# Kernel tuning notes

Measured on AMD Instinct MI355X. Metric: run time of the kernel, lower is better.

The kernel has to match this reference:

```python
import jax, jax.numpy as jnp
import numpy as np

N_NODES = 50000
N_EDGES = 800000
IN_SIZE = 128
NUM_HEADS = 8
HEAD_DIM = IN_SIZE // NUM_HEADS  # qk/val head dim = 16


def setup_inputs() -> dict:
    key = jax.random.key(0)
    ks = jax.random.split(key, 16)
    d = IN_SIZE
    lim = 1.0 / np.sqrt(d)
    inp = {
        "in_feats": jax.random.normal(ks[0], (N_NODES, d), jnp.float32),
        "struc_feats": jax.random.normal(ks[1], (N_NODES, d), jnp.float32),
        "edge_weights": jax.random.uniform(ks[2], (N_EDGES,), jnp.float32),
        "ln_scale": jnp.ones((d,), jnp.float32),
        "ln_bias": jnp.zeros((d,), jnp.float32),
        "Ws": jax.random.uniform(ks[3], (d, d), jnp.float32, -lim, lim),
        "bs": jnp.zeros((d,), jnp.float32),
        "Wq": jax.random.uniform(ks[4], (d, d), jnp.float32, -lim, lim),
        "bq": jnp.zeros((d,), jnp.float32),
        "Wk": jax.random.uniform(ks[5], (d, d), jnp.float32, -lim, lim),
        "bk": jnp.zeros((d,), jnp.float32),
        "Wv": jax.random.uniform(ks[6], (d, d), jnp.float32, -lim, lim),
        "bv": jnp.zeros((d,), jnp.float32),
        "Wo": jax.random.uniform(ks[7], (d, d), jnp.float32, -lim, lim),
        "edge_ids": jax.random.randint(ks[8], (2, N_EDGES), 0, N_NODES, jnp.int64)
        if jax.config.jax_enable_x64 else jax.random.randint(ks[8], (2, N_EDGES), 0, N_NODES, jnp.int32),
    }
    return inp


def _layer_norm(x, scale, bias, eps=1e-5):
    mu = jnp.mean(x, axis=-1, keepdims=True)
    var = jnp.var(x, axis=-1, keepdims=True)
    return (x - mu) * jax.lax.rsqrt(var + eps) * scale + bias


def reference(in_feats, struc_feats, edge_weights, ln_scale, ln_bias,
              Ws, bs, Wq, bq, Wk, bk, Wv, bv, Wo, edge_ids):
    N = in_feats.shape[0]
    H, hd = NUM_HEADS, HEAD_DIM

    delta = _layer_norm(in_feats, ln_scale, ln_bias)           # pre-norm
    delta = jax.nn.gelu(delta, approximate=False)               # pre-activation (exact GELU, torch default)
    delta_struc = delta + struc_feats @ Ws.T + bs               # struc_proj add

    qry = (delta_struc @ Wq.T + bq) / np.sqrt(hd)                # [N, qk]
    keyf = delta_struc @ Wk.T + bk                               # [N, qk]
    val = delta @ Wv.T + bv                                      # [N, val]

    src, dst = edge_ids[0], edge_ids[1]                          # out[src] += A[src,dst] * val[dst]
    qe = qry[src].reshape(-1, H, hd)                             # [E, H, hd]
    ke = keyf[dst].reshape(-1, H, hd)                            # [E, H, hd]
    attn = jax.nn.sigmoid(jnp.sum(qe * ke, axis=-1))             # [E, H]
    attn = edge_weights[:, None] * attn

    msgs = attn[:, :, None] * val[dst].reshape(-1, H, hd)        # [E, H, hd]
    agg = jax.ops.segment_sum(msgs.reshape(-1, H * hd), src, num_segments=N)  # [N, val]

    out = agg @ Wo.T                                             # out_proj (no bias)
    return in_feats + out                                        # skip connection
```

## Files before the change

### kernel.cpp

```cpp
#include <hip/hip_runtime.h>
#include <math.h>

#define NF 128

typedef __attribute__((ext_vector_type(8))) short short8;
typedef __attribute__((ext_vector_type(4))) float floatx4;

__device__ __forceinline__ unsigned short f2bf(float f) {
    union { float x; unsigned int i; } c; c.x = f;
    unsigned int r = c.i + 0x7fffu + ((c.i >> 16) & 1u);
    return (unsigned short)(r >> 16);
}
__device__ __forceinline__ float bf2f(unsigned short u) {
    union { unsigned int i; float x; } c; c.i = ((unsigned int)u) << 16;
    return c.x;
}
__device__ __forceinline__ void unpack8(uint4 u, float* f) {
    union { unsigned int i; float x; } c;
    c.i = u.x << 16;          f[0] = c.x;
    c.i = u.x & 0xffff0000u;  f[1] = c.x;
    c.i = u.y << 16;          f[2] = c.x;
    c.i = u.y & 0xffff0000u;  f[3] = c.x;
    c.i = u.z << 16;          f[4] = c.x;
    c.i = u.z & 0xffff0000u;  f[5] = c.x;
    c.i = u.w << 16;          f[6] = c.x;
    c.i = u.w & 0xffff0000u;  f[7] = c.x;
}
__device__ __forceinline__ ushort4 pack4(float a, float b, float c, float d) {
    ushort4 h; h.x = f2bf(a); h.y = f2bf(b); h.z = f2bf(c); h.w = f2bf(d);
    return h;
}

__global__ __launch_bounds__(256) void wconv5_kernel(
    const float* __restrict__ a, const float* __restrict__ b,
    const float* __restrict__ c, const float* __restrict__ d,
    const float* __restrict__ e, unsigned short* __restrict__ o)
{
    int i = blockIdx.x * 256 + threadIdx.x;
    int w = i >> 14, j = i & 16383;
    const float* p = (w == 0) ? a : (w == 1) ? b : (w == 2) ? c : (w == 3) ? d : e;
    o[i] = f2bf(p[j]);
}

__global__ __launch_bounds__(256) void node_a_kernel(
    const float* __restrict__ in_feats, const float* __restrict__ struc,
    const float* __restrict__ gamma, const float* __restrict__ beta,
    const unsigned short* __restrict__ Wsb, const float* __restrict__ bs,
    unsigned short* __restrict__ deltab, unsigned short* __restrict__ dstrb, int M)
{
    __shared__ unsigned short Xd[64][136];
    __shared__ unsigned short Xs2[64][136];
    __shared__ unsigned short Wl[64][136];

    int tid = threadIdx.x;
    int m0 = blockIdx.x * 64;
    int lane = tid & 63, w = tid >> 6, lg = lane & 15, quad = lane >> 4;

    {
        const uint4* g = (const uint4*)Wsb;
        #pragma unroll
        for (int p = 0; p < 4; ++p) {
            int idx = tid + p * 256;
            *(uint4*)&Wl[idx >> 4][(idx & 15) * 8] = g[idx];
        }
    }
    {
        int row = tid >> 2, t4 = tid & 3;
        int gm = m0 + row;
        bool vr = gm < M;
        const float4* ip = (const float4*)(in_feats + (size_t)gm * NF) + t4 * 8;
        float4 xf[8];
        #pragma unroll
        for (int p = 0; p < 8; ++p)
            xf[p] = vr ? ip[p] : make_float4(0.f, 0.f, 0.f, 0.f);
        float s = 0.f, sq = 0.f;
        #pragma unroll
        for (int p = 0; p < 8; ++p) {
            s  += xf[p].x + xf[p].y + xf[p].z + xf[p].w;
            sq += xf[p].x * xf[p].x + xf[p].y * xf[p].y
                + xf[p].z * xf[p].z + xf[p].w * xf[p].w;
        }
        s  += __shfl_xor(s, 1, 64);  s  += __shfl_xor(s, 2, 64);
        sq += __shfl_xor(sq, 1, 64); sq += __shfl_xor(sq, 2, 64);
        float mu = s * (1.0f / 128.0f);
        float var = sq * (1.0f / 128.0f) - mu * mu;
        float rstd = rsqrtf(var + 1e-5f);
        const float4* gp = (const float4*)gamma + t4 * 8;
        const float4* bp = (const float4*)beta + t4 * 8;
        #pragma unroll
        for (int p = 0; p < 8; ++p) {
            float4 g4 = gp[p], b4 = bp[p];
            float o0 = (xf[p].x - mu) * rstd * g4.x + b4.x;
            float o1 = (xf[p].y - mu) * rstd * g4.y + b4.y;
            float o2 = (xf[p].z - mu) * rstd * g4.z + b4.z;
            float o3 = (xf[p].w - mu) * rstd * g4.w + b4.w;
            o0 = 0.5f * o0 * (1.0f + erff(o0 * 0.70710678118654752f));
            o1 = 0.5f * o1 * (1.0f + erff(o1 * 0.70710678118654752f));
            o2 = 0.5f * o2 * (1.0f + erff(o2 * 0.70710678118654752f));
            o3 = 0.5f * o3 * (1.0f + erff(o3 * 0.70710678118654752f));
            *(ushort4*)&Xd[row][t4 * 32 + p * 4] = pack4(o0, o1, o2, o3);
        }
        const float4* sp = (const float4*)(struc + (size_t)gm * NF) + t4 * 8;
        #pragma unroll
        for (int p = 0; p < 8; ++p) {
            float4 f = vr ? sp[p] : make_float4(0.f, 0.f, 0.f, 0.f);
            *(ushort4*)&Xs2[row][t4 * 32 + p * 4] = pack4(f.x, f.y, f.z, f.w);
        }
    }
    __syncthreads();

    floatx4 acc[8];
    #pragma unroll
    for (int t = 0; t < 8; ++t) acc[t] = (floatx4){0.f, 0.f, 0.f, 0.f};

    #pragma unroll
    for (int ks = 0; ks < 4; ++ks) {
        short8 a = *(const short8*)&Xs2[w * 16 + lg][ks * 32 + quad * 8];
        #pragma unroll
        for (int t = 0; t < 4; ++t) {
            short8 b = *(const short8*)&Wl[t * 16 + lg][ks * 32 + quad * 8];
            acc[t] = __builtin_amdgcn_mfma_f32_16x16x32_bf16(a, b, acc[t], 0, 0, 0);
        }
    }
    __syncthreads();
    {
        const uint4* g = (const uint4*)(Wsb + 8192);
        #pragma unroll
        for (int p = 0; p < 4; ++p) {
            int idx = tid + p * 256;
            *(uint4*)&Wl[idx >> 4][(idx & 15) * 8] = g[idx];
        }
    }
    __syncthreads();
    #pragma unroll
    for (int ks = 0; ks < 4; ++ks) {
        short8 a = *(const short8*)&Xs2[w * 16 + lg][ks * 32 + quad * 8];
        #pragma unroll
        for (int t = 0; t < 4; ++t) {
            short8 b = *(const short8*)&Wl[t * 16 + lg][ks * 32 + quad * 8];
            acc[4 + t] = __builtin_amdgcn_mfma_f32_16x16x32_bf16(a, b, acc[4 + t], 0, 0, 0);
        }
    }

    #pragma unroll
    for (int t = 0; t < 8; ++t) {
        int col = t * 16 + lg;
        float bvv = bs[col];
        #pragma unroll
        for (int r = 0; r < 4; ++r) {
            int rl = w * 16 + quad * 4 + r;
            Xs2[rl][col] = f2bf(acc[t][r] + bvv + bf2f(Xd[rl][col]));
        }
    }
    #pragma unroll
    for (int p = 0; p < 4; ++p) {
        int idx = lane + p * 64;
        int row = w * 16 + (idx >> 4), c16 = idx & 15;
        int gm = m0 + row;
        if (gm < M) {
            *(uint4*)(deltab + (size_t)gm * NF + c16 * 8) = *(const uint4*)&Xd[row][c16 * 8];
            *(uint4*)(dstrb  + (size_t)gm * NF + c16 * 8) = *(const uint4*)&Xs2[row][c16 * 8];
        }
    }
}

__global__ __launch_bounds__(256) void node_qkv_kernel(
    const unsigned short* __restrict__ deltab, const unsigned short* __restrict__ dstrb,
    const unsigned short* __restrict__ Wall, const float* __restrict__ bq,
    const float* __restrict__ bk, const float* __restrict__ bv,
    unsigned short* __restrict__ qb, unsigned short* __restrict__ kb,
    unsigned short* __restrict__ vb, int M)
{
    __shared__ unsigned short Xs[64][136];
    __shared__ unsigned short Wl[128][136];

    int tid = threadIdx.x;
    int m0 = blockIdx.x * 64;
    int y = blockIdx.y;
    int lane = tid & 63, w = tid >> 6, lg = lane & 15, quad = lane >> 4;

    const unsigned short* Xg = (y == 2) ? deltab : dstrb;
    const unsigned short* Wg = Wall + (y + 1) * 16384;
    const float* bias = (y == 0) ? bq : (y == 1) ? bk : bv;
    float scale = (y == 0) ? 0.25f : 1.0f;
    unsigned short* outg = (y == 0) ? qb : (y == 1) ? kb : vb;

    {
        const uint4* g = (const uint4*)Wg;
        #pragma unroll
        for (int p = 0; p < 8; ++p) {
            int idx = tid + p * 256;
            *(uint4*)&Wl[idx >> 4][(idx & 15) * 8] = g[idx];
        }
    }
    {
        const uint4* X = (const uint4*)Xg;
        #pragma unroll
        for (int p = 0; p < 4; ++p) {
            int idx = lane + p * 64;
            int row = w * 16 + (idx >> 4), c16 = idx & 15;
            int gm = m0 + row;
            uint4 u = make_uint4(0u, 0u, 0u, 0u);
            if (gm < M) u = X[(size_t)gm * 16 + c16];
            *(uint4*)&Xs[row][c16 * 8] = u;
        }
    }
    __syncthreads();

    floatx4 acc[8];
    #pragma unroll
    for (int t = 0; t < 8; ++t) acc[t] = (floatx4){0.f, 0.f, 0.f, 0.f};
    #pragma unroll
    for (int ks = 0; ks < 4; ++ks) {
        short8 a = *(const short8*)&Xs[w * 16 + lg][ks * 32 + quad * 8];
        #pragma unroll
        for (int t = 0; t < 8; ++t) {
            short8 b = *(const short8*)&Wl[t * 16 + lg][ks * 32 + quad * 8];
            acc[t] = __builtin_amdgcn_mfma_f32_16x16x32_bf16(a, b, acc[t], 0, 0, 0);
        }
    }

    #pragma unroll
    for (int t = 0; t < 8; ++t) {
        int col = t * 16 + lg;
        float bvv = bias[col];
        #pragma unroll
        for (int r = 0; r < 4; ++r)
            Xs[w * 16 + quad * 4 + r][col] = f2bf((acc[t][r] + bvv) * scale);
    }
    #pragma unroll
    for (int p = 0; p < 4; ++p) {
        int idx = lane + p * 64;
        int row = w * 16 + (idx >> 4), c16 = idx & 15;
        int gm = m0 + row;
        if (gm < M)
            *(uint4*)(outg + (size_t)gm * NF + c16 * 8) = *(const uint4*)&Xs[row][c16 * 8];
    }
}

__global__ __launch_bounds__(256) void gemm_out_kernel(
    const unsigned short* __restrict__ Xb, const unsigned short* __restrict__ Wb,
    const float* __restrict__ addf, float* __restrict__ Y, int M)
{
    __shared__ unsigned short Xs[64][136];
    __shared__ unsigned short Wl[128][136];
    int tid = threadIdx.x;
    int m0 = blockIdx.x * 64;
    int lane = tid & 63, w = tid >> 6, lg = lane & 15, quad = lane >> 4;

    {
        const uint4* g = (const uint4*)Wb;
        #pragma unroll
        for (int p = 0; p < 8; ++p) {
            int idx = tid + p * 256;
            *(uint4*)&Wl[idx >> 4][(idx & 15) * 8] = g[idx];
        }
    }
    {
        const uint4* X = (const uint4*)Xb;
        #pragma unroll
        for (int p = 0; p < 4; ++p) {
            int idx = lane + p * 64;
            int row = w * 16 + (idx >> 4), c16 = idx & 15;
            int gm = m0 + row;
            uint4 u = make_uint4(0u, 0u, 0u, 0u);
            if (gm < M) u = X[(size_t)gm * 16 + c16];
            *(uint4*)&Xs[row][c16 * 8] = u;
        }
    }
    __syncthreads();

    floatx4 acc[8];
    #pragma unroll
    for (int t = 0; t < 8; ++t) acc[t] = (floatx4){0.f, 0.f, 0.f, 0.f};
    #pragma unroll
    for (int ks = 0; ks < 4; ++ks) {
        short8 a = *(const short8*)&Xs[w * 16 + lg][ks * 32 + quad * 8];
        #pragma unroll
        for (int t = 0; t < 8; ++t) {
            short8 b = *(const short8*)&Wl[t * 16 + lg][ks * 32 + quad * 8];
            acc[t] = __builtin_amdgcn_mfma_f32_16x16x32_bf16(a, b, acc[t], 0, 0, 0);
        }
    }
    #pragma unroll
    for (int t = 0; t < 8; ++t) {
        int col = t * 16 + lg;
        #pragma unroll
        for (int r = 0; r < 4; ++r) {
            int gm = m0 + w * 16 + quad * 4 + r;
            if (gm >= M) continue;
            size_t off = (size_t)gm * NF + col;
            Y[off] = acc[t][r] + addf[off];
        }
    }
}

__global__ void hist_kernel(const int* __restrict__ eid, int* __restrict__ cnt, int E)
{
    int i = blockIdx.x * blockDim.x + threadIdx.x;
    if (i < E) atomicAdd(&cnt[eid[i]], 1);
}

__global__ __launch_bounds__(256) void scan1_kernel(
    const int* __restrict__ cnt, int* __restrict__ bsum, int n)
{
    int base = blockIdx.x * 1024;
    int s = 0;
    #pragma unroll
    for (int p = 0; p < 4; ++p) {
        int i = base + (int)threadIdx.x + p * 256;
        if (i < n) s += cnt[i];
    }
    #pragma unroll
    for (int m = 1; m <= 32; m <<= 1) s += __shfl_xor(s, m, 64);
    __shared__ int ws_[4];
    int wid = threadIdx.x >> 6;
    if ((threadIdx.x & 63) == 0) ws_[wid] = s;
    __syncthreads();
    if (threadIdx.x == 0) bsum[blockIdx.x] = ws_[0] + ws_[1] + ws_[2] + ws_[3];
}

__global__ __launch_bounds__(256) void scan3_kernel(
    const int* __restrict__ cnt, const int* __restrict__ bsum,
    int* __restrict__ row_start, int* __restrict__ cursor, int n, int nb)
{
    __shared__ int base_off;
    int tid = threadIdx.x, lane = tid & 63, wid = tid >> 6;
    if (tid == 0) {
        int a = 0;
        for (int j = 0; j < (int)blockIdx.x; ++j) a += bsum[j];
        base_off = a;
        if ((int)blockIdx.x == nb - 1) {
            int tot = a;
            for (int j = blockIdx.x; j < nb; ++j) tot += bsum[j];
            row_start[n] = tot;
        }
    }
    int base = blockIdx.x * 1024;
    int v[4]; int s = 0;
    #pragma unroll
    for (int p = 0; p < 4; ++p) {
        int i = base + tid * 4 + p;
        v[p] = (i < n) ? cnt[i] : 0;
        s += v[p];
    }
    int ss = s;
    #pragma unroll
    for (int off = 1; off < 64; off <<= 1) {
        int t = __shfl_up(ss, off, 64);
        if (lane >= off) ss += t;
    }
    __shared__ int wsum[4];
    if (lane == 63) wsum[wid] = ss;
    __syncthreads();
    int woff = 0;
    for (int j = 0; j < wid; ++j) woff += wsum[j];
    int a = base_off + woff + (ss - s);
    #pragma unroll
    for (int p = 0; p < 4; ++p) {
        int i = base + tid * 4 + p;
        if (i < n) { row_start[i] = a; cursor[i] = a; a += v[p]; }
    }
}

__global__ void scatter_kernel(const int* __restrict__ eid, const float* __restrict__ ew,
                               int* __restrict__ cursor, int2* __restrict__ edata, int E)
{
    int i = blockIdx.x * blockDim.x + threadIdx.x;
    if (i < E) {
        int src = eid[i];
        int dst = eid[E + i];
        int pos = atomicAdd(&cursor[src], 1);
        edata[pos] = make_int2(dst, __float_as_int(ew[i]));
    }
}

__global__ __launch_bounds__(256) void aggregate_kernel(
    const unsigned short* __restrict__ Q, const unsigned short* __restrict__ Kf,
    const unsigned short* __restrict__ V, const int* __restrict__ row_start,
    const int2* __restrict__ edata, unsigned short* __restrict__ agg, int N)
{
    int node = blockIdx.x * 4 + (threadIdx.x >> 6);
    if (node >= N) return;
    int lane = threadIdx.x & 63;
    int sg = lane >> 4, lg = lane & 15;
    int rs = row_start[node], re = row_start[node + 1];

    float qv[8];
    unpack8(*(const uint4*)(Q + (size_t)node * NF + lg * 8), qv);
    float acc[8];
    #pragma unroll
    for (int j = 0; j < 8; ++j) acc[j] = 0.f;

    int e1 = rs + sg, e2 = rs + sg + 4;
    int2 ed1 = (e1 < re) ? edata[e1] : make_int2(0, 0);
    int2 ed2 = (e2 < re) ? edata[e2] : make_int2(0, 0);

    for (int e0 = rs; e0 < re; e0 += 8) {
        int2 c1 = ed1, c2 = ed2;
        int en1 = e0 + 8 + sg, en2 = en1 + 4;
        ed1 = (en1 < re) ? edata[en1] : make_int2(0, 0);
        ed2 = (en2 < re) ? edata[en2] : make_int2(0, 0);

        float kv1[8], kv2[8];
        unpack8(*(const uint4*)(Kf + (size_t)c1.x * NF + lg * 8), kv1);
        unpack8(*(const uint4*)(Kf + (size_t)c2.x * NF + lg * 8), kv2);
        float s1 = qv[0] * kv1[0], s2 = qv[0] * kv2[0];
        #pragma unroll
        for (int j = 1; j < 8; ++j) {
            s1 = fmaf(qv[j], kv1[j], s1);
            s2 = fmaf(qv[j], kv2[j], s2);
        }
        s1 += __shfl_xor(s1, 1, 64);
        s2 += __shfl_xor(s2, 1, 64);
        float a1 = __int_as_float(c1.y) / (1.f + __expf(-s1));
        float a2 = __int_as_float(c2.y) / (1.f + __expf(-s2));

        float vv1[8], vv2[8];
        unpack8(*(const uint4*)(V + (size_t)c1.x * NF + lg * 8), vv1);
        unpack8(*(const uint4*)(V + (size_t)c2.x * NF + lg * 8), vv2);
        #pragma unroll
        for (int j = 0; j < 8; ++j) {
            acc[j] = fmaf(a1, vv1[j], acc[j]);
            acc[j] = fmaf(a2, vv2[j], acc[j]);
        }
    }
    #pragma unroll
    for (int j = 0; j < 8; ++j) {
        acc[j] += __shfl_xor(acc[j], 16, 64);
        acc[j] += __shfl_xor(acc[j], 32, 64);
    }
    if (sg == 0) {
        unsigned short* o = agg + (size_t)node * NF + lg * 8;
        *(ushort4*)o       = pack4(acc[0], acc[1], acc[2], acc[3]);
        *(ushort4*)(o + 4) = pack4(acc[4], acc[5], acc[6], acc[7]);
    }
}

extern "C" void kernel_launch(void* const* d_in, const int* in_sizes, int n_in,
                              void* d_out, int out_size, void* d_ws, size_t ws_size,
                              hipStream_t stream)
{
    const float* in_feats = (const float*)d_in[0];
    const float* struc    = (const float*)d_in[1];
    const float* eweights = (const float*)d_in[2];
    const float* ln_scale = (const float*)d_in[3];
    const float* ln_bias  = (const float*)d_in[4];
    const float* Ws       = (const float*)d_in[5];
    const float* bs       = (const float*)d_in[6];
    const float* Wq       = (const float*)d_in[7];
    const float* bq       = (const float*)d_in[8];
    const float* Wk       = (const float*)d_in[9];
    const float* bk       = (const float*)d_in[10];
    const float* Wv       = (const float*)d_in[11];
    const float* bv       = (const float*)d_in[12];
    const float* Wo       = (const float*)d_in[13];
    const int*   edge_ids = (const int*)d_in[14];
    float* out = (float*)d_out;

    int N = in_sizes[0] / NF;
    int E = in_sizes[2];

    size_t F = (size_t)N * NF;
    unsigned short* deltab = (unsigned short*)d_ws;
    unsigned short* dstrb  = deltab + F;
    unsigned short* qb     = dstrb + F;
    unsigned short* kb     = qb + F;
    unsigned short* vb     = kb + F;
    unsigned short* aggb   = vb + F;
    unsigned short* Wall   = aggb + F;
    int2*  edata     = (int2*)(Wall + 5 * 16384);
    int*   cnt       = (int*)(edata + E);
    int*   row_start = cnt + N;
    int*   cursor    = row_start + N + 1;
    int*   bsum      = cursor + N;

    int gb  = (N + 63) / 64;
    int geb = (E + 255) / 256;
    int nb  = (N + 1023) / 1024;

    wconv5_kernel<<<(5 * 16384) / 256, 256, 0, stream>>>(Ws, Wq, Wk, Wv, Wo, Wall);

    hipMemsetAsync(cnt, 0, (size_t)N * sizeof(int), stream);
    hist_kernel<<<geb, 256, 0, stream>>>(edge_ids, cnt, E);
    scan1_kernel<<<nb, 256, 0, stream>>>(cnt, bsum, N);
    scan3_kernel<<<nb, 256, 0, stream>>>(cnt, bsum, row_start, cursor, N, nb);
    scatter_kernel<<<geb, 256, 0, stream>>>(edge_ids, eweights, cursor, edata, E);

    node_a_kernel<<<gb, 256, 0, stream>>>(in_feats, struc, ln_scale, ln_bias,
                                          Wall, bs, deltab, dstrb, N);
    node_qkv_kernel<<<dim3(gb, 3), 256, 0, stream>>>(deltab, dstrb, Wall,
                                                     bq, bk, bv, qb, kb, vb, N);

    aggregate_kernel<<<(N + 3) / 4, 256, 0, stream>>>(qb, kb, vb, row_start, edata, aggb, N);

    gemm_out_kernel<<<gb, 256, 0, stream>>>(aggb, Wall + 4 * 16384, in_feats, out, N);
}
```

Measured before the change: 337.5 us.

## Persistent-tile GEMM kernels with resident weights and interleaved K/V layout

Turns the node GEMM kernels into persistent grid-stride loops, so each block loads the 128x128 bf16 weight matrix into LDS once and reuses it across many 64-row tiles. A operands now go straight from global memory into registers instead of being staged through LDS. K and V are stored interleaved per node, so the aggregation gathers both from one 512-byte row and gets better locality on random neighbor accesses. Costs include fixed grid sizes tuned to the device, more LDS per block in node_a, and missing barriers between tile iterations that reuse Xs2/Cst, which could race.

```diff
diff --git a/kernel.cpp b/kernel.cpp
--- a/kernel.cpp
+++ b/kernel.cpp
@@ -46,120 +46,118 @@
     const float* __restrict__ in_feats, const float* __restrict__ struc,
     const float* __restrict__ gamma, const float* __restrict__ beta,
     const unsigned short* __restrict__ Wsb, const float* __restrict__ bs,
-    unsigned short* __restrict__ deltab, unsigned short* __restrict__ dstrb, int M)
-{
-    __shared__ unsigned short Xd[64][136];
+    unsigned short* __restrict__ deltab, unsigned short* __restrict__ dstrb,
+    int M, int nt)
+{
+    __shared__ unsigned short Wl[128][136];
     __shared__ unsigned short Xs2[64][136];
-    __shared__ unsigned short Wl[64][136];
 
     int tid = threadIdx.x;
-    int m0 = blockIdx.x * 64;
     int lane = tid & 63, w = tid >> 6, lg = lane & 15, quad = lane >> 4;
+    int lrow = tid >> 2, t4 = tid & 3;
 
     {
         const uint4* g = (const uint4*)Wsb;
         #pragma unroll
-        for (int p = 0; p < 4; ++p) {
+        for (int p = 0; p < 8; ++p) {
             int idx = tid + p * 256;
             *(uint4*)&Wl[idx >> 4][(idx & 15) * 8] = g[idx];
         }
     }
-    {
-        int row = tid >> 2, t4 = tid & 3;
-        int gm = m0 + row;
+    float bsr[8];
+    #pragma unroll
+    for (int t = 0; t < 8; ++t) bsr[t] = bs[t * 16 + lg];
+    __syncthreads();
+
+    for (int tile = blockIdx.x; tile < nt; tile += gridDim.x) {
+        int m0 = tile * 64;
+        int gm = m0 + lrow;
         bool vr = gm < M;
-        const float4* ip = (const float4*)(in_feats + (size_t)gm * NF) + t4 * 8;
-        float4 xf[8];
-        #pragma unroll
-        for (int p = 0; p < 8; ++p)
-            xf[p] = vr ? ip[p] : make_float4(0.f, 0.f, 0.f, 0.f);
-        float s = 0.f, sq = 0.f;
-        #pragma unroll
-        for (int p = 0; p < 8; ++p) {
-            s  += xf[p].x + xf[p].y + xf[p].z + xf[p].w;
-            sq += xf[p].x * xf[p].x + xf[p].y * xf[p].y
-                + xf[p].z * xf[p].z + xf[p].w * xf[p].w;
-        }
-        s  += __shfl_xor(s, 1, 64);  s  += __shfl_xor(s, 2, 64);
-        sq += __shfl_xor(sq, 1, 64); sq += __shfl_xor(sq, 2, 64);
-        float mu = s * (1.0f / 128.0f);
-        float var = sq * (1.0f / 128.0f) - mu * mu;
-        float rstd = rsqrtf(var + 1e-5f);
-        const float4* gp = (const float4*)gamma + t4 * 8;
-        const float4* bp = (const float4*)beta + t4 * 8;
-        #pragma unroll
-        for (int p = 0; p < 8; ++p) {
-            float4 g4 = gp[p], b4 = bp[p];
-            float o0 = (xf[p].x - mu) * rstd * g4.x + b4.x;
-            float o1 = (xf[p].y - mu) * rstd * g4.y + b4.y;
-            float o2 = (xf[p].z - mu) * rstd * g4.z + b4.z;
-            float o3 = (xf[p].w - mu) * rstd * g4.w + b4.w;
-            o0 = 0.5f * o0 * (1.0f + erff(o0 * 0.70710678118654752f));
-            o1 = 0.5f * o1 * (1.0f + erff(o1 * 0.70710678118654752f));
-            o2 = 0.5f * o2 * (1.0f + erff(o2 * 0.70710678118654752f));
-            o3 = 0.5f * o3 * (1.0f + erff(o3 * 0.70710678118654752f));
-            *(ushort4*)&Xd[row][t4 * 32 + p * 4] = pack4(o0, o1, o2, o3);
-        }
-        const float4* sp = (const float4*)(struc + (size_t)gm * NF) + t4 * 8;
-        #pragma unroll
-        for (int p = 0; p < 8; ++p) {
-            float4 f = vr ? sp[p] : make_float4(0.f, 0.f, 0.f, 0.f);
-            *(ushort4*)&Xs2[row][t4 * 32 + p * 4] = pack4(f.x, f.y, f.z, f.w);
-        }
-    }
-    __syncthreads();
-
-    floatx4 acc[8];
-    #pragma unroll
-    for (int t = 0; t < 8; ++t) acc[t] = (floatx4){0.f, 0.f, 0.f, 0.f};
-
-    #pragma unroll
-    for (int ks = 0; ks < 4; ++ks) {
-        short8 a = *(const short8*)&Xs2[w * 16 + lg][ks * 32 + quad * 8];
-        #pragma unroll
-        for (int t = 0; t < 4; ++t) {
-            short8 b = *(const short8*)&Wl[t * 16 + lg][ks * 32 + quad * 8];
-            acc[t] = __builtin_amdgcn_mfma_f32_16x16x32_bf16(a, b, acc[t], 0, 0, 0);
-        }
-    }
-    __syncthreads();
-    {
-        const uint4* g = (const uint4*)(Wsb + 8192);
+        size_t rbase = (size_t)(vr ? gm : 0) * NF;
+
+        uint dreg[16];
+        {
+            const float4* ip = (const float4*)(in_feats + rbase) + t4 * 8;
+            float4 xf[8];
+            #pragma unroll
+            for (int p = 0; p < 8; ++p) xf[p] = ip[p];
+            float s = 0.f, sq = 0.f;
+            #pragma unroll
+            for (int p = 0; p < 8; ++p) {
+                s  += xf[p].x + xf[p].y + xf[p].z + xf[p].w;
+                sq += xf[p].x * xf[p].x + xf[p].y * xf[p].y
+                    + xf[p].z * xf[p].z + xf[p].w * xf[p].w;
+            }
+            s  += __shfl_xor(s, 1, 64);  s  += __shfl_xor(s, 2, 64);
+            sq += __shfl_xor(sq, 1, 64); sq += __shfl_xor(sq, 2, 64);
+            float mu = s * (1.0f / 128.0f);
+            float var = sq * (1.0f / 128.0f) - mu * mu;
+            float rstd = rsqrtf(var + 1e-5f);
+            const float4* gp = (const float4*)gamma + t4 * 8;
+            const float4* bp = (const float4*)beta + t4 * 8;
+            #pragma unroll
+            for (int p = 0; p < 8; ++p) {
+                float4 g4 = gp[p], b4 = bp[p];
+                float o0 = (xf[p].x - mu) * rstd * g4.x + b4.x;
+                float o1 = (xf[p].y - mu) * rstd * g4.y + b4.y;
+                float o2 = (xf[p].z - mu) * rstd * g4.z + b4.z;
+                float o3 = (xf[p].w - mu) * rstd * g4.w + b4.w;
+                o0 = 0.5f * o0 * (1.0f + erff(o0 * 0.70710678118654752f));
+                o1 = 0.5f * o1 * (1.0f + erff(o1 * 0.70710678118654752f));
+                o2 = 0.5f * o2 * (1.0f + erff(o2 * 0.70710678118654752f));
+                o3 = 0.5f * o3 * (1.0f + erff(o3 * 0.70710678118654752f));
+                ushort4 h = pack4(o0, o1, o2, o3);
+                dreg[p * 2]     = (uint)h.x | ((uint)h.y << 16);
+                dreg[p * 2 + 1] = (uint)h.z | ((uint)h.w << 16);
+            }
+            if (vr) {
+                uint4* od = (uint4*)(deltab + (size_t)gm * NF + t4 * 32);
+                #pragma unroll
+                for (int q = 0; q < 4; ++q)
+                    od[q] = make_uint4(dreg[q*4], dreg[q*4+1], dreg[q*4+2], dreg[q*4+3]);
+            }
+            const float4* sp = (const float4*)(struc + rbase) + t4 * 8;
+            #pragma unroll
+            for (int p = 0; p < 8; ++p) {
+                float4 f = sp[p];
+                *(ushort4*)&Xs2[lrow][t4 * 32 + p * 4] = pack4(f.x, f.y, f.z, f.w);
+            }
+        }
+
+        floatx4 acc[8];
+        #pragma unroll
+        for (int t = 0; t < 8; ++t) acc[t] = (floatx4){0.f, 0.f, 0.f, 0.f};
+        #pragma unroll
+        for (int ks = 0; ks < 4; ++ks) {
+            short8 a = *(const short8*)&Xs2[w * 16 + lg][ks * 32 + quad * 8];
+            #pragma unroll
+            for (int t = 0; t < 8; ++t) {
+                short8 b = *(const short8*)&Wl[t * 16 + lg][ks * 32 + quad * 8];
+                acc[t] = __builtin_amdgcn_mfma_f32_16x16x32_bf16(a, b, acc[t], 0, 0, 0);
+            }
+        }
+
+        #pragma unroll
+        for (int q = 0; q < 4; ++q)
+            *(uint4*)&Xs2[lrow][t4 * 32 + q * 8] =
+                make_uint4(dreg[q*4], dreg[q*4+1], dreg[q*4+2], dreg[q*4+3]);
+
+        #pragma unroll
+        for (int t = 0; t < 8; ++t) {
+            int col = t * 16 + lg;
+            #pragma unroll
+            for (int r = 0; r < 4; ++r) {
+                int rl = w * 16 + quad * 4 + r;
+                Xs2[rl][col] = f2bf(acc[t][r] + bsr[t] + bf2f(Xs2[rl][col]));
+            }
+        }
         #pragma unroll
         for (int p = 0; p < 4; ++p) {
-            int idx = tid + p * 256;
-            *(uint4*)&Wl[idx >> 4][(idx & 15) * 8] = g[idx];
-        }
-    }
-    __syncthreads();
-    #pragma unroll
-    for (int ks = 0; ks < 4; ++ks) {
-        short8 a = *(const short8*)&Xs2[w * 16 + lg][ks * 32 + quad * 8];
-        #pragma unroll
-        for (int t = 0; t < 4; ++t) {
-            short8 b = *(const short8*)&Wl[t * 16 + lg][ks * 32 + quad * 8];
-            acc[4 + t] = __builtin_amdgcn_mfma_f32_16x16x32_bf16(a, b, acc[4 + t], 0, 0, 0);
-        }
-    }
-
-    #pragma unroll
-    for (int t = 0; t < 8; ++t) {
-        int col = t * 16 + lg;
-        float bvv = bs[col];
-        #pragma unroll
-        for (int r = 0; r < 4; ++r) {
-            int rl = w * 16 + quad * 4 + r;
-            Xs2[rl][col] = f2bf(acc[t][r] + bvv + bf2f(Xd[rl][col]));
-        }
-    }
-    #pragma unroll
-    for (int p = 0; p < 4; ++p) {
-        int idx = lane + p * 64;
-        int row = w * 16 + (idx >> 4), c16 = idx & 15;
-        int gm = m0 + row;
-        if (gm < M) {
-            *(uint4*)(deltab + (size_t)gm * NF + c16 * 8) = *(const uint4*)&Xd[row][c16 * 8];
-            *(uint4*)(dstrb  + (size_t)gm * NF + c16 * 8) = *(const uint4*)&Xs2[row][c16 * 8];
+            int idx = lane + p * 64;
+            int row = w * 16 + (idx >> 4), c16 = idx & 15;
+            int gmo = m0 + row;
+            if (gmo < M)
+                *(uint4*)(dstrb + (size_t)gmo * NF + c16 * 8) = *(const uint4*)&Xs2[row][c16 * 8];
         }
     }
 }
@@ -168,14 +166,13 @@
     const unsigned short* __restrict__ deltab, const unsigned short* __restrict__ dstrb,
     const unsigned short* __restrict__ Wall, const float* __restrict__ bq,
     const float* __restrict__ bk, const float* __restrict__ bv,
-    unsigned short* __restrict__ qb, unsigned short* __restrict__ kb,
-    unsigned short* __restrict__ vb, int M)
-{
-    __shared__ unsigned short Xs[64][136];
+    unsigned short* __restrict__ qb, unsigned short* __restrict__ kvb,
+    int M, int nt)
+{
     __shared__ unsigned short Wl[128][136];
+    __shared__ unsigned short Cst[64][136];
 
     int tid = threadIdx.x;
-    int m0 = blockIdx.x * 64;
     int y = blockIdx.y;
     int lane = tid & 63, w = tid >> 6, lg = lane & 15, quad = lane >> 4;
 
@@ -183,7 +180,8 @@
     const unsigned short* Wg = Wall + (y + 1) * 16384;
     const float* bias = (y == 0) ? bq : (y == 1) ? bk : bv;
     float scale = (y == 0) ? 0.25f : 1.0f;
-    unsigned short* outg = (y == 0) ? qb : (y == 1) ? kb : vb;
+    unsigned short* outg = (y == 0) ? qb : (y == 1) ? kvb : (kvb + NF);
+    int ostride = (y == 0) ? NF : 2 * NF;
 
     {
         const uint4* g = (const uint4*)Wg;
@@ -193,59 +191,54 @@
             *(uint4*)&Wl[idx >> 4][(idx & 15) * 8] = g[idx];
         }
     }
-    {
-        const uint4* X = (const uint4*)Xg;
+    float br[8];
+    #pragma unroll
+    for (int t = 0; t < 8; ++t) br[t] = bias[t * 16 + lg] * scale;
+    __syncthreads();
+
+    for (int tile = blockIdx.x; tile < nt; tile += gridDim.x) {
+        int m0 = tile * 64;
+        int am = m0 + w * 16 + lg;
+        const unsigned short* arow = Xg + (size_t)(am < M ? am : 0) * NF + quad * 8;
+
+        floatx4 acc[8];
+        #pragma unroll
+        for (int t = 0; t < 8; ++t) acc[t] = (floatx4){0.f, 0.f, 0.f, 0.f};
+        short8 af[4];
+        #pragma unroll
+        for (int ks = 0; ks < 4; ++ks) af[ks] = *(const short8*)(arow + ks * 32);
+        #pragma unroll
+        for (int ks = 0; ks < 4; ++ks) {
+            #pragma unroll
+            for (int t = 0; t < 8; ++t) {
+                short8 b = *(const short8*)&Wl[t * 16 + lg][ks * 32 + quad * 8];
+                acc[t] = __builtin_amdgcn_mfma_f32_16x16x32_bf16(af[ks], b, acc[t], 0, 0, 0);
+            }
+        }
+        #pragma unroll
+        for (int t = 0; t < 8; ++t) {
+            int col = t * 16 + lg;
+            #pragma unroll
+            for (int r = 0; r < 4; ++r)
+                Cst[w * 16 + quad * 4 + r][col] = f2bf(acc[t][r] * scale + br[t]);
+        }
         #pragma unroll
         for (int p = 0; p < 4; ++p) {
             int idx = lane + p * 64;
             int row = w * 16 + (idx >> 4), c16 = idx & 15;
             int gm = m0 + row;
-            uint4 u = make_uint4(0u, 0u, 0u, 0u);
-            if (gm < M) u = X[(size_t)gm * 16 + c16];
-            *(uint4*)&Xs[row][c16 * 8] = u;
-        }
-    }
-    __syncthreads();
-
-    floatx4 acc[8];
-    #pragma unroll
-    for (int t = 0; t < 8; ++t) acc[t] = (floatx4){0.f, 0.f, 0.f, 0.f};
-    #pragma unroll
-    for (int ks = 0; ks < 4; ++ks) {
-        short8 a = *(const short8*)&Xs[w * 16 + lg][ks * 32 + quad * 8];
-        #pragma unroll
-        for (int t = 0; t < 8; ++t) {
-            short8 b = *(const short8*)&Wl[t * 16 + lg][ks * 32 + quad * 8];
-            acc[t] = __builtin_amdgcn_mfma_f32_16x16x32_bf16(a, b, acc[t], 0, 0, 0);
-        }
-    }
-
-    #pragma unroll
-    for (int t = 0; t < 8; ++t) {
-        int col = t * 16 + lg;
-        float bvv = bias[col];
-        #pragma unroll
-        for (int r = 0; r < 4; ++r)
-            Xs[w * 16 + quad * 4 + r][col] = f2bf((acc[t][r] + bvv) * scale);
-    }
-    #pragma unroll
-    for (int p = 0; p < 4; ++p) {
-        int idx = lane + p * 64;
-        int row = w * 16 + (idx >> 4), c16 = idx & 15;
-        int gm = m0 + row;
-        if (gm < M)
-            *(uint4*)(outg + (size_t)gm * NF + c16 * 8) = *(const uint4*)&Xs[row][c16 * 8];
+            if (gm < M)
+                *(uint4*)(outg + (size_t)gm * ostride + c16 * 8) = *(const uint4*)&Cst[row][c16 * 8];
+        }
     }
 }
 
 __global__ __launch_bounds__(256) void gemm_out_kernel(
     const unsigned short* __restrict__ Xb, const unsigned short* __restrict__ Wb,
-    const float* __restrict__ addf, float* __restrict__ Y, int M)
-{
-    __shared__ unsigned short Xs[64][136];
+    const float* __restrict__ addf, float* __restrict__ Y, int M, int nt)
+{
     __shared__ unsigned short Wl[128][136];
     int tid = threadIdx.x;
-    int m0 = blockIdx.x * 64;
     int lane = tid & 63, w = tid >> 6, lg = lane & 15, quad = lane >> 4;
 
     {
@@ -256,41 +249,37 @@
             *(uint4*)&Wl[idx >> 4][(idx & 15) * 8] = g[idx];
         }
     }
-    {
-        const uint4* X = (const uint4*)Xb;
-        #pragma unroll
-        for (int p = 0; p < 4; ++p) {
-            int idx = lane + p * 64;
-            int row = w * 16 + (idx >> 4), c16 = idx & 15;
-            int gm = m0 + row;
-            uint4 u = make_uint4(0u, 0u, 0u, 0u);
-            if (gm < M) u = X[(size_t)gm * 16 + c16];
-            *(uint4*)&Xs[row][c16 * 8] = u;
-        }
-    }
     __syncthreads();
 
-    floatx4 acc[8];
-    #pragma unroll
-    for (int t = 0; t < 8; ++t) acc[t] = (floatx4){0.f, 0.f, 0.f, 0.f};
-    #pragma unroll
-    for (int ks = 0; ks < 4; ++ks) {
-        short8 a = *(const short8*)&Xs[w * 16 + lg][ks * 32 + quad * 8];
+    for (int tile = blockIdx.x; tile < nt; tile += gridDim.x) {
+        int m0 = tile * 64;
+        int am = m0 + w * 16 + lg;
+        const unsigned short* arow = Xb + (size_t)(am < M ? am : 0) * NF + quad * 8;
+
+        floatx4 acc[8];
+        #pragma unroll
+        for (int t = 0; t < 8; ++t) acc[t] = (floatx4){0.f, 0.f, 0.f, 0.f};
+        short8 af[4];
+        #pragma unroll
+        for (int ks = 0; ks < 4; ++ks) af[ks] = *(const short8*)(arow + ks * 32);
+        #pragma unroll
+        for (int ks = 0; ks < 4; ++ks) {
+            #pragma unroll
+            for (int t = 0; t < 8; ++t) {
+                short8 b = *(const short8*)&Wl[t * 16 + lg][ks * 32 + quad * 8];
+                acc[t] = __builtin_amdgcn_mfma_f32_16x16x32_bf16(af[ks], b, acc[t], 0, 0, 0);
+            }
+        }
         #pragma unroll
         for (int t = 0; t < 8; ++t) {
-            short8 b = *(const short8*)&Wl[t * 16 + lg][ks * 32 + quad * 8];
-            acc[t] = __builtin_amdgcn_mfma_f32_16x16x32_bf16(a, b, acc[t], 0, 0, 0);
-        }
-    }
-    #pragma unroll
-    for (int t = 0; t < 8; ++t) {
-        int col = t * 16 + lg;
-        #pragma unroll
-        for (int r = 0; r < 4; ++r) {
-            int gm = m0 + w * 16 + quad * 4 + r;
-            if (gm >= M) continue;
-            size_t off = (size_t)gm * NF + col;
-            Y[off] = acc[t][r] + addf[off];
+            int col = t * 16 + lg;
+            #pragma unroll
+            for (int r = 0; r < 4; ++r) {
+                int gm = m0 + w * 16 + quad * 4 + r;
+                if (gm >= M) continue;
+                size_t off = (size_t)gm * NF + col;
+                Y[off] = acc[t][r] + addf[off];
+            }
         }
     }
 }
@@ -376,9 +365,9 @@
 }
 
 __global__ __launch_bounds__(256) void aggregate_kernel(
-    const unsigned short* __restrict__ Q, const unsigned short* __restrict__ Kf,
-    const unsigned short* __restrict__ V, const int* __restrict__ row_start,
-    const int2* __restrict__ edata, unsigned short* __restrict__ agg, int N)
+    const unsigned short* __restrict__ Q, const unsigned short* __restrict__ kvb,
+    const int* __restrict__ row_start, const int2* __restrict__ edata,
+    unsigned short* __restrict__ agg, int N)
 {
     int node = blockIdx.x * 4 + (threadIdx.x >> 6);
     if (node >= N) return;
@@ -402,9 +391,14 @@
         ed1 = (en1 < re) ? edata[en1] : make_int2(0, 0);
         ed2 = (en2 < re) ? edata[en2] : make_int2(0, 0);
 
+        const uint4* p1 = (const uint4*)kvb + (size_t)c1.x * 32 + lg;
+        const uint4* p2 = (const uint4*)kvb + (size_t)c2.x * 32 + lg;
+        uint4 k1u = p1[0], v1u = p1[16];
+        uint4 k2u = p2[0], v2u = p2[16];
+
         float kv1[8], kv2[8];
-        unpack8(*(const uint4*)(Kf + (size_t)c1.x * NF + lg * 8), kv1);
-        unpack8(*(const uint4*)(Kf + (size_t)c2.x * NF + lg * 8), kv2);
+        unpack8(k1u, kv1);
+        unpack8(k2u, kv2);
         float s1 = qv[0] * kv1[0], s2 = qv[0] * kv2[0];
         #pragma unroll
         for (int j = 1; j < 8; ++j) {
@@ -417,8 +411,8 @@
         float a2 = __int_as_float(c2.y) / (1.f + __expf(-s2));
 
         float vv1[8], vv2[8];
-        unpack8(*(const uint4*)(V + (size_t)c1.x * NF + lg * 8), vv1);
-        unpack8(*(const uint4*)(V + (size_t)c2.x * NF + lg * 8), vv2);
+        unpack8(v1u, vv1);
+        unpack8(v2u, vv2);
         #pragma unroll
         for (int j = 0; j < 8; ++j) {
             acc[j] = fmaf(a1, vv1[j], acc[j]);
@@ -465,9 +459,8 @@
     unsigned short* deltab = (unsigned short*)d_ws;
     unsigned short* dstrb  = deltab + F;
     unsigned short* qb     = dstrb + F;
-    unsigned short* kb     = qb + F;
-    unsigned short* vb     = kb + F;
-    unsigned short* aggb   = vb + F;
+    unsigned short* kvb    = qb + F;
+    unsigned short* aggb   = kvb + 2 * F;
     unsigned short* Wall   = aggb + F;
     int2*  edata     = (int2*)(Wall + 5 * 16384);
     int*   cnt       = (int*)(edata + E);
@@ -475,7 +468,7 @@
     int*   cursor    = row_start + N + 1;
     int*   bsum      = cursor + N;
 
-    int gb  = (N + 63) / 64;
+    int nt  = (N + 63) / 64;
     int geb = (E + 255) / 256;
     int nb  = (N + 1023) / 1024;
 
@@ -487,12 +480,12 @@
     scan3_kernel<<<nb, 256, 0, stream>>>(cnt, bsum, row_start, cursor, N, nb);
     scatter_kernel<<<geb, 256, 0, stream>>>(edge_ids, eweights, cursor, edata, E);
 
-    node_a_kernel<<<gb, 256, 0, stream>>>(in_feats, struc, ln_scale, ln_bias,
-                                          Wall, bs, deltab, dstrb, N);
-    node_qkv_kernel<<<dim3(gb, 3), 256, 0, stream>>>(deltab, dstrb, Wall,
-                                                     bq, bk, bv, qb, kb, vb, N);
-
-    aggregate_kernel<<<(N + 3) / 4, 256, 0, stream>>>(qb, kb, vb, row_start, edata, aggb, N);
-
-    gemm_out_kernel<<<gb, 256, 0, stream>>>(aggb, Wall + 4 * 16384, in_feats, out, N);
-}
+    node_a_kernel<<<392, 256, 0, stream>>>(in_feats, struc, ln_scale, ln_bias,
+                                           Wall, bs, deltab, dstrb, N, nt);
+    node_qkv_kernel<<<dim3(261, 3), 256, 0, stream>>>(deltab, dstrb, Wall,
+                                                      bq, bk, bv, qb, kvb, N, nt);
+
+    aggregate_kernel<<<(N + 3) / 4, 256, 0, stream>>>(qb, kvb, row_start, edata, aggb, N);
+
+    gemm_out_kernel<<<392, 256, 0, stream>>>(aggb, Wall + 4 * 16384, in_feats, out, N, nt);
+}
```

After: 326.1 us. 1.03x faster.
